# Kernel tuning notes

Hardware: AMD Instinct MI355X
Metric: run time of the kernel (lower is better)

## Reference

```python
import jax, jax.numpy as jnp
import numpy as np

N, T, F, H = 20000, 64, 32, 64
E = 640000
G1, G2 = 64, 32


def _lstm_layer(x_seq, Wih, Whh, bih, bhh):
    # x_seq: [N, T, Fin] -> hs [N, T, H], PyTorch gate order i,f,g,o
    n, _, _ = x_seq.shape
    h_dim = Whh.shape[1]
    h0 = jnp.zeros((n, h_dim), x_seq.dtype)
    c0 = jnp.zeros((n, h_dim), x_seq.dtype)

    def step(carry, xt):
        h, c = carry
        gates = xt @ Wih.T + h @ Whh.T + bih + bhh
        i, f, g, o = jnp.split(gates, 4, axis=-1)
        c = jax.nn.sigmoid(f) * c + jax.nn.sigmoid(i) * jnp.tanh(g)
        h = jax.nn.sigmoid(o) * jnp.tanh(c)
        return (h, c), h

    (_, _), hs = jax.lax.scan(step, (h0, c0), jnp.swapaxes(x_seq, 0, 1))
    return jnp.swapaxes(hs, 0, 1)


def _gcn(h, src, dst, W, b):
    # GCNConv (PyG default): add self-loops, symmetric deg^-1/2 normalization
    n = h.shape[0]
    loop = jnp.arange(n)
    s = jnp.concatenate([src, loop])
    d = jnp.concatenate([dst, loop])
    deg = jax.ops.segment_sum(jnp.ones_like(d, dtype=h.dtype), d, num_segments=n)
    dinv = jnp.where(deg > 0, deg ** -0.5, 0.0)
    norm = dinv[s] * dinv[d]
    xw = h @ W                      # [n, out]
    msg = xw[s] * norm[:, None]     # gather on source nodes
    return jax.ops.segment_sum(msg, d, num_segments=n) + b


def setup_inputs() -> dict:
    key = jax.random.key(0)
    ks = jax.random.split(key, 16)
    s = 0.1
    inp = {
        "x": jax.random.normal(ks[0], (N, T, F), jnp.float32),
        "stock_ids": jax.random.randint(ks[1], (N,), 0, N),
        "edge_index": jax.random.randint(ks[2], (2, E), 0, N),
        # LSTM layer 0
        "Wih0": jax.random.normal(ks[3], (4 * H, F), jnp.float32) * s,
        "Whh0": jax.random.normal(ks[4], (4 * H, H), jnp.float32) * s,
        "bih0": jnp.zeros((4 * H,), jnp.float32),
        "bhh0": jnp.zeros((4 * H,), jnp.float32),
        # LSTM layer 1
        "Wih1": jax.random.normal(ks[5], (4 * H, H), jnp.float32) * s,
        "Whh1": jax.random.normal(ks[6], (4 * H, H), jnp.float32) * s,
        "bih1": jnp.zeros((4 * H,), jnp.float32),
        "bhh1": jnp.zeros((4 * H,), jnp.float32),
        # GCN layers
        "gcn1_W": jax.random.normal(ks[7], (H, G1), jnp.float32) * s,
        "gcn1_b": jnp.zeros((G1,), jnp.float32),
        "gcn2_W": jax.random.normal(ks[8], (G1, G2), jnp.float32) * s,
        "gcn2_b": jnp.zeros((G2,), jnp.float32),
        # head
        "fc_W": jax.random.normal(ks[9], (1, G2), jnp.float32) * s,
        "fc_b": jnp.zeros((1,), jnp.float32),
    }
    return inp


def reference(x, stock_ids, edge_index, Wih0, Whh0, bih0, bhh0,
              Wih1, Whh1, bih1, bhh1, gcn1_W, gcn1_b, gcn2_W, gcn2_b,
              fc_W, fc_b):
    # 2-layer LSTM (eval mode: inter-layer dropout is identity)
    h1 = _lstm_layer(x, Wih0, Whh0, bih0, bhh0)
    h2 = _lstm_layer(h1, Wih1, Whh1, bih1, bhh1)
    h = h2[:, -1, :]                              # [N, H]
    src, dst = edge_index[0], edge_index[1]
    g = jax.nn.relu(_gcn(h, src, dst, gcn1_W, gcn1_b))
    g = jax.nn.relu(_gcn(g, src, dst, gcn2_W, gcn2_b))
    node_features = g[stock_ids]                  # [B, 32]
    out = node_features @ fc_W.T + fc_b           # [B, 1]
    return out.squeeze(-1)
```

## Files before the change

### kernel.cpp

```cpp
#include <hip/hip_runtime.h>
#include <math.h>

#define TT 64
#define FF 32
#define HH 64
#define NN 16
#define GG1 64
#define GG2 32

typedef float f32x4 __attribute__((ext_vector_type(4)));
typedef short bf16x8 __attribute__((ext_vector_type(8)));

__device__ __forceinline__ float fexp2(float x){ return __builtin_amdgcn_exp2f(x); }
__device__ __forceinline__ float frcp (float x){ return __builtin_amdgcn_rcpf(x); }
#define L2E 1.442695041f
__device__ __forceinline__ float sigm_nb(float v, float nb){
  return frcp(1.0f + fexp2(fmaf(v, -L2E, nb)));
}
__device__ __forceinline__ float tanh_b(float v, float b2){
  return fmaf(-2.0f, frcp(1.0f + fexp2(fmaf(v, 2.0f*L2E, b2))), 1.0f);
}
__device__ __forceinline__ float tanh0(float v){
  return fmaf(-2.0f, frcp(1.0f + fexp2(2.0f*L2E*v)), 1.0f);
}

__device__ __forceinline__ float xor8(float v){
  int a = __builtin_bit_cast(int, v);
  int b = __builtin_amdgcn_update_dpp(0, a, 0x128, 0xF, 0xF, true);
  return __builtin_bit_cast(float, b);
}

__device__ __forceinline__ unsigned short bf16rn(float x){
  unsigned u = __builtin_bit_cast(unsigned, x);
  return (unsigned short)((u + 0x7FFFu + ((u >> 16) & 1u)) >> 16);
}
__device__ __forceinline__ void split2(float x, unsigned short& h, unsigned short& l){
  unsigned u = __builtin_bit_cast(unsigned, x);
  unsigned hr = (u + 0x7FFFu + ((u >> 16) & 1u)) & 0xFFFF0000u;
  h = (unsigned short)(hr >> 16);
  l = bf16rn(x - __builtin_bit_cast(float, hr));
}
__device__ __forceinline__ void split_pk(float a, float b, unsigned& hi2, unsigned& lo2){
  asm("v_cvt_pk_bf16_f32 %0, %1, %2" : "=v"(hi2) : "v"(a), "v"(b));
  float ha = __builtin_bit_cast(float, hi2 << 16);
  float hb = __builtin_bit_cast(float, hi2 & 0xFFFF0000u);
  float la = a - ha, lb = b - hb;
  asm("v_cvt_pk_bf16_f32 %0, %1, %2" : "=v"(lo2) : "v"(la), "v"(lb));
}

#define PIN(v) asm volatile("" : "+v"(v))
#define MFMA(acc, a, b) (acc) = __builtin_amdgcn_mfma_f32_16x16x32_bf16((a), (b), (acc), 0, 0, 0)

__device__ __forceinline__ void wsplit(const float* p, bf16x8& hi, bf16x8& lo){
  float4 a = *(const float4*)p;
  float4 b = *(const float4*)(p + 4);
  unsigned short h, s;
  split2(a.x,h,s); hi[0]=(short)h; lo[0]=(short)s;
  split2(a.y,h,s); hi[1]=(short)h; lo[1]=(short)s;
  split2(a.z,h,s); hi[2]=(short)h; lo[2]=(short)s;
  split2(a.w,h,s); hi[3]=(short)h; lo[3]=(short)s;
  split2(b.x,h,s); hi[4]=(short)h; lo[4]=(short)s;
  split2(b.y,h,s); hi[5]=(short)h; lo[5]=(short)s;
  split2(b.z,h,s); hi[6]=(short)h; lo[6]=(short)s;
  split2(b.w,h,s); hi[7]=(short)h; lo[7]=(short)s;
}

__global__ __launch_bounds__(512, 2)
void lstm_mfma(const float* __restrict__ x,
    const float* __restrict__ Wih0, const float* __restrict__ Whh0,
    const float* __restrict__ bih0, const float* __restrict__ bhh0,
    const float* __restrict__ Wih1, const float* __restrict__ Whh1,
    const float* __restrict__ bih1, const float* __restrict__ bhh1,
    float* __restrict__ hout, int n)
{
  const int tid = threadIdx.x;
  const int w   = tid >> 6;
  const int l   = tid & 63;
  const int lr  = l & 15;
  const int lg  = l >> 4;
  const int nA  = blockIdx.x * NN;
  int avail = n - nA; if (avail > NN) avail = NN;

  __shared__ short Ax[2][2][16][40];
  __shared__ short H0[2][2][16][88];
  __shared__ short H1[2][2][16][88];

  const int jm   = lr & 7;
  const bool lo8 = (lr < 8);
  const int col0 = lo8 ? (8*w + jm) : (64  + 8*w + jm);
  const int col1 = lo8 ? (128 + 8*w + jm) : (192 + 8*w + jm);

  bf16x8 W0h[2][3], W0l[2][3], W1h[2][4], W1l[2][4];
#pragma unroll
  for (int h = 0; h < 2; ++h){
    const int col = h ? col1 : col0;
    wsplit(Wih0 + col*FF + 8*lg,      W0h[h][0], W0l[h][0]);
    wsplit(Whh0 + col*HH + 8*lg,      W0h[h][1], W0l[h][1]);
    wsplit(Whh0 + col*HH + 32 + 8*lg, W0h[h][2], W0l[h][2]);
    wsplit(Wih1 + col*HH + 8*lg,      W1h[h][0], W1l[h][0]);
    wsplit(Wih1 + col*HH + 32 + 8*lg, W1h[h][1], W1l[h][1]);
    wsplit(Whh1 + col*HH + 8*lg,      W1h[h][2], W1l[h][2]);
    wsplit(Whh1 + col*HH + 32 + 8*lg, W1h[h][3], W1l[h][3]);
  }
#pragma unroll
  for (int h = 0; h < 2; ++h){
#pragma unroll
    for (int k = 0; k < 3; ++k){ PIN(W0h[h][k]); PIN(W0l[h][k]); }
#pragma unroll
    for (int k = 0; k < 4; ++k){ PIN(W1h[h][k]); PIN(W1l[h][k]); }
  }

  const int m  = 8*w + jm;
  const float nb_i0 = -L2E      * (bih0[m      ] + bhh0[m      ]);
  const float nb_f0 = -L2E      * (bih0[m +  64] + bhh0[m +  64]);
  const float b2_g0 =  2.0f*L2E * (bih0[m + 128] + bhh0[m + 128]);
  const float nb_o0 = -L2E      * (bih0[m + 192] + bhh0[m + 192]);
  const float nb_i1 = -L2E      * (bih1[m      ] + bhh1[m      ]);
  const float nb_f1 = -L2E      * (bih1[m +  64] + bhh1[m +  64]);
  const float b2_g1 =  2.0f*L2E * (bih1[m + 128] + bhh1[m + 128]);
  const float nb_o1 = -L2E      * (bih1[m + 192] + bhh1[m + 192]);

  {
    short* p0 = &H0[0][0][0][0];
    short* p1 = &H1[0][0][0][0];
    for (int i = tid; i < 2*2*16*88; i += 512){ p0[i] = 0; p1[i] = 0; }
    const int xnd = tid >> 5, xf = tid & 31;
    float v = (xnd < avail) ? x[((size_t)(nA+xnd)*TT + 0)*FF + xf] : 0.0f;
    unsigned short hh, hl; split2(v, hh, hl);
    Ax[0][0][xnd][xf] = (short)hh;
    Ax[0][1][xnd][xf] = (short)hl;
  }
  const int na = 4*lg + (lo8 ? 0 : 2);
  const int nb = na + 1;
  float c0a = 0.0f, c0b = 0.0f, c1a = 0.0f, c1b = 0.0f;
  const f32x4 Z = {0.f, 0.f, 0.f, 0.f};
  __syncthreads();

  for (int t = 0; t < TT; ++t){
    const int rd0 = (t & 1) ^ 1;
    const int wr0 =  t & 1;
    const int rd1 =  t & 1;
    const int wr1 = (t & 1) ^ 1;

    const int xnd = tid >> 5, xf = tid & 31;
    const int tp = t + 1;
    float xv = 0.0f;
    if (tp < TT && xnd < avail) xv = x[((size_t)(nA+xnd)*TT + tp)*FF + xf];

    bf16x8 axh  = *(const bf16x8*)&Ax[t&1][0][lr][8*lg];
    bf16x8 axl  = *(const bf16x8*)&Ax[t&1][1][lr][8*lg];
    bf16x8 h0ah = *(const bf16x8*)&H0[rd0][0][lr][8*lg];
    bf16x8 h0al = *(const bf16x8*)&H0[rd0][1][lr][8*lg];
    bf16x8 h0bh = *(const bf16x8*)&H0[rd0][0][lr][32+8*lg];
    bf16x8 h0bl = *(const bf16x8*)&H0[rd0][1][lr][32+8*lg];

    __builtin_amdgcn_s_setprio(1);
    f32x4 acc0, acc1;
    acc0 = __builtin_amdgcn_mfma_f32_16x16x32_bf16(axl, W0h[0][0], Z, 0, 0, 0);
    acc1 = __builtin_amdgcn_mfma_f32_16x16x32_bf16(axl, W0h[1][0], Z, 0, 0, 0);
    MFMA(acc0, axh,  W0l[0][0]); MFMA(acc0, axh,  W0h[0][0]);
    MFMA(acc1, axh,  W0l[1][0]); MFMA(acc1, axh,  W0h[1][0]);
    MFMA(acc0, h0al, W0h[0][1]); MFMA(acc0, h0ah, W0l[0][1]); MFMA(acc0, h0ah, W0h[0][1]);
    MFMA(acc1, h0al, W0h[1][1]); MFMA(acc1, h0ah, W0l[1][1]); MFMA(acc1, h0ah, W0h[1][1]);
    MFMA(acc0, h0bl, W0h[0][2]); MFMA(acc0, h0bh, W0l[0][2]); MFMA(acc0, h0bh, W0h[0][2]);
    MFMA(acc1, h0bl, W0h[1][2]); MFMA(acc1, h0bh, W0l[1][2]); MFMA(acc1, h0bh, W0h[1][2]);

    f32x4 acd0, acd1;
    if (t > 0){
      bf16x8 h1ah = *(const bf16x8*)&H1[rd1][0][lr][8*lg];
      bf16x8 h1al = *(const bf16x8*)&H1[rd1][1][lr][8*lg];
      bf16x8 h1bh = *(const bf16x8*)&H1[rd1][0][lr][32+8*lg];
      bf16x8 h1bl = *(const bf16x8*)&H1[rd1][1][lr][32+8*lg];
      acd0 = __builtin_amdgcn_mfma_f32_16x16x32_bf16(h0al, W1h[0][0], Z, 0, 0, 0);
      acd1 = __builtin_amdgcn_mfma_f32_16x16x32_bf16(h0al, W1h[1][0], Z, 0, 0, 0);
      MFMA(acd0, h0ah, W1l[0][0]); MFMA(acd0, h0ah, W1h[0][0]);
      MFMA(acd1, h0ah, W1l[1][0]); MFMA(acd1, h0ah, W1h[1][0]);
      MFMA(acd0, h0bl, W1h[0][1]); MFMA(acd0, h0bh, W1l[0][1]); MFMA(acd0, h0bh, W1h[0][1]);
      MFMA(acd1, h0bl, W1h[1][1]); MFMA(acd1, h0bh, W1l[1][1]); MFMA(acd1, h0bh, W1h[1][1]);
      MFMA(acd0, h1al, W1h[0][2]); MFMA(acd0, h1ah, W1l[0][2]); MFMA(acd0, h1ah, W1h[0][2]);
      MFMA(acd1, h1al, W1h[1][2]); MFMA(acd1, h1ah, W1l[1][2]); MFMA(acd1, h1ah, W1h[1][2]);
      MFMA(acd0, h1bl, W1h[0][3]); MFMA(acd0, h1bh, W1l[0][3]); MFMA(acd0, h1bh, W1h[0][3]);
      MFMA(acd1, h1bl, W1h[1][3]); MFMA(acd1, h1bh, W1l[1][3]); MFMA(acd1, h1bh, W1h[1][3]);
    }
    __builtin_amdgcn_s_setprio(0);

    if (tp < TT){
      unsigned short hh, hl; split2(xv, hh, hl);
      Ax[tp&1][0][xnd][xf] = (short)hh;
      Ax[tp&1][1][xnd][xf] = (short)hl;
    }

    {
      f32x4 s0, s1;
      s0[0]=xor8(acc0[0]); s0[1]=xor8(acc0[1]); s0[2]=xor8(acc0[2]); s0[3]=xor8(acc0[3]);
      s1[0]=xor8(acc1[0]); s1[1]=xor8(acc1[1]); s1[2]=xor8(acc1[2]); s1[3]=xor8(acc1[3]);
      float gi_a = lo8 ? acc0[0] : s0[2],  gi_b = lo8 ? acc0[1] : s0[3];
      float gf_a = lo8 ? s0[0] : acc0[2],  gf_b = lo8 ? s0[1] : acc0[3];
      float gg_a = lo8 ? acc1[0] : s1[2],  gg_b = lo8 ? acc1[1] : s1[3];
      float go_a = lo8 ? s1[0] : acc1[2],  go_b = lo8 ? s1[1] : acc1[3];
      c0a = sigm_nb(gf_a, nb_f0)*c0a + sigm_nb(gi_a, nb_i0)*tanh_b(gg_a, b2_g0);
      float ha = sigm_nb(go_a, nb_o0)*tanh0(c0a);
      c0b = sigm_nb(gf_b, nb_f0)*c0b + sigm_nb(gi_b, nb_i0)*tanh_b(gg_b, b2_g0);
      float hb = sigm_nb(go_b, nb_o0)*tanh0(c0b);
      unsigned hi2, lo2; split_pk(ha, hb, hi2, lo2);
      H0[wr0][0][na][m] = (short)(hi2 & 0xFFFF);
      H0[wr0][0][nb][m] = (short)(hi2 >> 16);
      H0[wr0][1][na][m] = (short)(lo2 & 0xFFFF);
      H0[wr0][1][nb][m] = (short)(lo2 >> 16);
    }
    if (t > 0){
      f32x4 s0, s1;
      s0[0]=xor8(acd0[0]); s0[1]=xor8(acd0[1]); s0[2]=xor8(acd0[2]); s0[3]=xor8(acd0[3]);
      s1[0]=xor8(acd1[0]); s1[1]=xor8(acd1[1]); s1[2]=xor8(acd1[2]); s1[3]=xor8(acd1[3]);
      float gi_a = lo8 ? acd0[0] : s0[2],  gi_b = lo8 ? acd0[1] : s0[3];
      float gf_a = lo8 ? s0[0] : acd0[2],  gf_b = lo8 ? s0[1] : acd0[3];
      float gg_a = lo8 ? acd1[0] : s1[2],  gg_b = lo8 ? acd1[1] : s1[3];
      float go_a = lo8 ? s1[0] : acd1[2],  go_b = lo8 ? s1[1] : acd1[3];
      c1a = sigm_nb(gf_a, nb_f1)*c1a + sigm_nb(gi_a, nb_i1)*tanh_b(gg_a, b2_g1);
      float ha = sigm_nb(go_a, nb_o1)*tanh0(c1a);
      c1b = sigm_nb(gf_b, nb_f1)*c1b + sigm_nb(gi_b, nb_i1)*tanh_b(gg_b, b2_g1);
      float hb = sigm_nb(go_b, nb_o1)*tanh0(c1b);
      unsigned hi2, lo2; split_pk(ha, hb, hi2, lo2);
      H1[wr1][0][na][m] = (short)(hi2 & 0xFFFF);
      H1[wr1][0][nb][m] = (short)(hi2 >> 16);
      H1[wr1][1][na][m] = (short)(lo2 & 0xFFFF);
      H1[wr1][1][nb][m] = (short)(lo2 >> 16);
    }
    __syncthreads();
  }

  {
    const int rd0 = (TT-1) & 1;
    const int rd1 =  TT & 1;
    bf16x8 h0ah = *(const bf16x8*)&H0[rd0][0][lr][8*lg];
    bf16x8 h0al = *(const bf16x8*)&H0[rd0][1][lr][8*lg];
    bf16x8 h0bh = *(const bf16x8*)&H0[rd0][0][lr][32+8*lg];
    bf16x8 h0bl = *(const bf16x8*)&H0[rd0][1][lr][32+8*lg];
    bf16x8 h1ah = *(const bf16x8*)&H1[rd1][0][lr][8*lg];
    bf16x8 h1al = *(const bf16x8*)&H1[rd1][1][lr][8*lg];
    bf16x8 h1bh = *(const bf16x8*)&H1[rd1][0][lr][32+8*lg];
    bf16x8 h1bl = *(const bf16x8*)&H1[rd1][1][lr][32+8*lg];
    f32x4 acd0 = __builtin_amdgcn_mfma_f32_16x16x32_bf16(h0al, W1h[0][0], Z, 0, 0, 0);
    f32x4 acd1 = __builtin_amdgcn_mfma_f32_16x16x32_bf16(h0al, W1h[1][0], Z, 0, 0, 0);
    MFMA(acd0, h0ah, W1l[0][0]); MFMA(acd0, h0ah, W1h[0][0]);
    MFMA(acd1, h0ah, W1l[1][0]); MFMA(acd1, h0ah, W1h[1][0]);
    MFMA(acd0, h0bl, W1h[0][1]); MFMA(acd0, h0bh, W1l[0][1]); MFMA(acd0, h0bh, W1h[0][1]);
    MFMA(acd1, h0bl, W1h[1][1]); MFMA(acd1, h0bh, W1l[1][1]); MFMA(acd1, h0bh, W1h[1][1]);
    MFMA(acd0, h1al, W1h[0][2]); MFMA(acd0, h1ah, W1l[0][2]); MFMA(acd0, h1ah, W1h[0][2]);
    MFMA(acd1, h1al, W1h[1][2]); MFMA(acd1, h1ah, W1l[1][2]); MFMA(acd1, h1ah, W1h[1][2]);
    MFMA(acd0, h1bl, W1h[0][3]); MFMA(acd0, h1bh, W1l[0][3]); MFMA(acd0, h1bh, W1h[0][3]);
    MFMA(acd1, h1bl, W1h[1][3]); MFMA(acd1, h1bh, W1l[1][3]); MFMA(acd1, h1bh, W1h[1][3]);

    f32x4 s0, s1;
    s0[0]=xor8(acd0[0]); s0[1]=xor8(acd0[1]); s0[2]=xor8(acd0[2]); s0[3]=xor8(acd0[3]);
    s1[0]=xor8(acd1[0]); s1[1]=xor8(acd1[1]); s1[2]=xor8(acd1[2]); s1[3]=xor8(acd1[3]);
    float gi_a = lo8 ? acd0[0] : s0[2],  gi_b = lo8 ? acd0[1] : s0[3];
    float gf_a = lo8 ? s0[0] : acd0[2],  gf_b = lo8 ? s0[1] : acd0[3];
    float gg_a = lo8 ? acd1[0] : s1[2],  gg_b = lo8 ? acd1[1] : s1[3];
    float go_a = lo8 ? s1[0] : acd1[2],  go_b = lo8 ? s1[1] : acd1[3];
    c1a = sigm_nb(gf_a, nb_f1)*c1a + sigm_nb(gi_a, nb_i1)*tanh_b(gg_a, b2_g1);
    float ha = sigm_nb(go_a, nb_o1)*tanh0(c1a);
    c1b = sigm_nb(gf_b, nb_f1)*c1b + sigm_nb(gi_b, nb_i1)*tanh_b(gg_b, b2_g1);
    float hb = sigm_nb(go_b, nb_o1)*tanh0(c1b);
    if (nA + na < n) hout[(size_t)(nA+na)*HH + m] = ha;
    if (nA + nb < n) hout[(size_t)(nA+nb)*HH + m] = hb;
  }
}

__global__ void k_count(const int* __restrict__ dst, int E, int* __restrict__ cnt)
{
  int e = blockIdx.x * blockDim.x + threadIdx.x;
  if (e < E) atomicAdd(&cnt[dst[e]], 1);
}

__global__ void k_scan_build(const int* __restrict__ cnt, int n,
                             int* __restrict__ offs, int* __restrict__ cursor,
                             float* __restrict__ dinv)
{
  __shared__ int part[1024];
  const int tid = threadIdx.x;
  const int per = (n + 1023) >> 10;
  const int base = tid * per;
  int s = 0;
  for (int i = 0; i < per; ++i) { int idx = base + i; if (idx < n) s += cnt[idx]; }
  part[tid] = s;
  __syncthreads();
  for (int off = 1; off < 1024; off <<= 1) {
    int v = 0;
    if (tid >= off) v = part[tid - off];
    __syncthreads();
    part[tid] += v;
    __syncthreads();
  }
  int run = part[tid] - s;
  for (int i = 0; i < per; ++i) {
    int idx = base + i;
    if (idx < n) {
      offs[idx] = run; cursor[idx] = run;
      int c = cnt[idx];
      dinv[idx] = 1.0f / sqrtf((float)(c + 1));
      run += c;
    }
  }
}

__global__ void k_fill(const int* __restrict__ src, const int* __restrict__ dst,
                       int E, int* __restrict__ cursor, int* __restrict__ csr)
{
  int e = blockIdx.x * blockDim.x + threadIdx.x;
  if (e < E) {
    int d = dst[e];
    int pos = atomicAdd(&cursor[d], 1);
    csr[pos] = src[e];
  }
}

template <int K, int M>
__global__ void k_xw(const float* __restrict__ A, const float* __restrict__ W,
                     float* __restrict__ out, int n)
{
  int idx = blockIdx.x * blockDim.x + threadIdx.x;
  int row = idx / M, col = idx % M;
  if (row >= n) return;
  const float* a = A + (size_t)row * K;
  float acc = 0.0f;
#pragma unroll
  for (int k = 0; k < K; ++k) acc = fmaf(a[k], W[k*M + col], acc);
  out[(size_t)row*M + col] = acc;
}

__global__ void k_agg_x2(const float* __restrict__ xw, const int* __restrict__ offs,
                         const int* __restrict__ cnt, const int* __restrict__ csr,
                         const float* __restrict__ dinv, const float* __restrict__ b,
                         const float* __restrict__ W2,
                         float* __restrict__ g1out, float* __restrict__ xw2out, int n)
{
  __shared__ float sg[4][GG1];
  const int nd   = threadIdx.x >> 6;
  const int lane = threadIdx.x & 63;
  const int node = blockIdx.x * 4 + nd;
  if (node < n) {
    const float di = dinv[node];
    float acc = xw[(size_t)node*GG1 + lane] * di * di;
    const int s0 = offs[node], e0 = s0 + cnt[node];
    for (int p = s0; p < e0; ++p) {
      int s = csr[p];
      acc = fmaf(xw[(size_t)s*GG1 + lane], dinv[s] * di, acc);
    }
    float val = fmaxf(acc + b[lane], 0.0f);
    g1out[(size_t)node*GG1 + lane] = val;
    sg[nd][lane] = val;
  }
  __syncthreads();
  if (node < n && lane < GG2) {
    float a2 = 0.0f;
#pragma unroll
    for (int k = 0; k < GG1; ++k) a2 = fmaf(sg[nd][k], W2[k*GG2 + lane], a2);
    xw2out[(size_t)node*GG2 + lane] = a2;
  }
}

template <int FD>
__global__ void k_agg(const float* __restrict__ xw, const int* __restrict__ offs,
                      const int* __restrict__ cnt, const int* __restrict__ csr,
                      const float* __restrict__ dinv, const float* __restrict__ b,
                      float* __restrict__ out, int n)
{
  int gidx = blockIdx.x * blockDim.x + threadIdx.x;
  int node = gidx / FD, lane = gidx % FD;
  if (node >= n) return;
  const float di = dinv[node];
  float acc = xw[(size_t)node*FD + lane] * di * di;
  const int s0 = offs[node], e0 = s0 + cnt[node];
  for (int p = s0; p < e0; ++p) {
    int s = csr[p];
    acc = fmaf(xw[(size_t)s*FD + lane], dinv[s] * di, acc);
  }
  out[(size_t)node*FD + lane] = fmaxf(acc + b[lane], 0.0f);
}

__global__ void k_fc(const float* __restrict__ g2, const int* __restrict__ sid,
                     const float* __restrict__ fcW, const float* __restrict__ fcb,
                     float* __restrict__ out, int n)
{
  int i = blockIdx.x * blockDim.x + threadIdx.x;
  if (i >= n) return;
  const float* row = g2 + (size_t)sid[i] * GG2;
  float acc = fcb[0];
#pragma unroll
  for (int f = 0; f < GG2; ++f) acc = fmaf(row[f], fcW[f], acc);
  out[i] = acc;
}

extern "C" void kernel_launch(void* const* d_in, const int* in_sizes, int n_in,
                              void* d_out, int out_size, void* d_ws, size_t ws_size,
                              hipStream_t stream)
{
  const float* x    = (const float*)d_in[0];
  const int*   sid  = (const int*)  d_in[1];
  const int*   eidx = (const int*)  d_in[2];
  const float* Wih0 = (const float*)d_in[3];
  const float* Whh0 = (const float*)d_in[4];
  const float* bih0 = (const float*)d_in[5];
  const float* bhh0 = (const float*)d_in[6];
  const float* Wih1 = (const float*)d_in[7];
  const float* Whh1 = (const float*)d_in[8];
  const float* bih1 = (const float*)d_in[9];
  const float* bhh1 = (const float*)d_in[10];
  const float* g1W  = (const float*)d_in[11];
  const float* g1b  = (const float*)d_in[12];
  const float* g2W  = (const float*)d_in[13];
  const float* g2b  = (const float*)d_in[14];
  const float* fcW  = (const float*)d_in[15];
  const float* fcb  = (const float*)d_in[16];

  const int n = in_sizes[1];
  const int E = in_sizes[2] / 2;
  float* out = (float*)d_out;

  char* w = (char*)d_ws;
  auto carve = [&](size_t bytes) -> void* {
    void* p = (void*)w; w += (bytes + 255) & ~(size_t)255; return p;
  };
  float* hfin   = (float*)carve((size_t)n * HH * 4);
  int*   cnt    = (int*)  carve((size_t)n * 4);
  int*   offs   = (int*)  carve((size_t)n * 4);
  int*   cursor = (int*)  carve((size_t)n * 4);
  float* dinv   = (float*)carve((size_t)n * 4);
  int*   csr    = (int*)  carve((size_t)E * 4);
  float* xw1    = (float*)carve((size_t)n * GG1 * 4);
  float* g1     = (float*)carve((size_t)n * GG1 * 4);
  float* xw2    = (float*)carve((size_t)n * GG2 * 4);
  float* g2     = (float*)carve((size_t)n * GG2 * 4);

  const int* src = eidx;
  const int* dst = eidx + E;

  lstm_mfma<<<(n + NN - 1) / NN, 512, 0, stream>>>(x, Wih0, Whh0, bih0, bhh0,
                                                   Wih1, Whh1, bih1, bhh1, hfin, n);

  hipMemsetAsync(cnt, 0, (size_t)n * 4, stream);
  k_count<<<(E + 255) / 256, 256, 0, stream>>>(dst, E, cnt);
  k_scan_build<<<1, 1024, 0, stream>>>(cnt, n, offs, cursor, dinv);
  k_fill<<<(E + 255) / 256, 256, 0, stream>>>(src, dst, E, cursor, csr);

  k_xw<HH, GG1><<<((size_t)n * GG1 + 255) / 256, 256, 0, stream>>>(hfin, g1W, xw1, n);
  k_agg_x2<<<(n + 3) / 4, 256, 0, stream>>>(xw1, offs, cnt, csr, dinv, g1b, g2W, g1, xw2, n);

  k_agg<GG2><<<((size_t)n * GG2 + 255) / 256, 256, 0, stream>>>(xw2, offs, cnt, csr, dinv, g2b, g2, n);

  k_fc<<<(n + 255) / 256, 256, 0, stream>>>(g2, sid, fcW, fcb, out, n);
}
```

Before: 696.5 us.

## Split LSTM layers across two wave groups in a 1024-thread block

The LSTM kernel now launches 1024 threads per block. Waves 0-7 compute layer 0 and waves 8-15 compute layer 1 (time-skewed by one step), so each wave holds only one layer's split weights in registers instead of both. This cuts per-thread register pressure and lets the two layers' MFMA chains run on different waves concurrently rather than serially in the same wave. The costs are a larger block barrier across 16 waves each step, and a tighter launch-bounds target (1024 threads, 4 blocks) that may force spills.

```diff
diff --git a/kernel.cpp b/kernel.cpp
--- a/kernel.cpp
+++ b/kernel.cpp
@@ -65,7 +65,7 @@
   split2(b.w,h,s); hi[7]=(short)h; lo[7]=(short)s;
 }
 
-__global__ __launch_bounds__(512, 2)
+__global__ __launch_bounds__(1024, 4)
 void lstm_mfma(const float* __restrict__ x,
     const float* __restrict__ Wih0, const float* __restrict__ Whh0,
     const float* __restrict__ bih0, const float* __restrict__ bhh0,
@@ -73,12 +73,14 @@
     const float* __restrict__ bih1, const float* __restrict__ bhh1,
     float* __restrict__ hout, int n)
 {
-  const int tid = threadIdx.x;
-  const int w   = tid >> 6;
-  const int l   = tid & 63;
-  const int lr  = l & 15;
-  const int lg  = l >> 4;
-  const int nA  = blockIdx.x * NN;
+  const int tid  = threadIdx.x;
+  const int wv   = tid >> 6;
+  const int role = wv >> 3;
+  const int w    = wv & 7;
+  const int l    = tid & 63;
+  const int lr   = l & 15;
+  const int lg   = l >> 4;
+  const int nA   = blockIdx.x * NN;
   int avail = n - nA; if (avail > NN) avail = NN;
 
   __shared__ short Ax[2][2][16][40];
@@ -90,49 +92,54 @@
   const int col0 = lo8 ? (8*w + jm) : (64  + 8*w + jm);
   const int col1 = lo8 ? (128 + 8*w + jm) : (192 + 8*w + jm);
 
-  bf16x8 W0h[2][3], W0l[2][3], W1h[2][4], W1l[2][4];
-#pragma unroll
-  for (int h = 0; h < 2; ++h){
-    const int col = h ? col1 : col0;
-    wsplit(Wih0 + col*FF + 8*lg,      W0h[h][0], W0l[h][0]);
-    wsplit(Whh0 + col*HH + 8*lg,      W0h[h][1], W0l[h][1]);
-    wsplit(Whh0 + col*HH + 32 + 8*lg, W0h[h][2], W0l[h][2]);
-    wsplit(Wih1 + col*HH + 8*lg,      W1h[h][0], W1l[h][0]);
-    wsplit(Wih1 + col*HH + 32 + 8*lg, W1h[h][1], W1l[h][1]);
-    wsplit(Whh1 + col*HH + 8*lg,      W1h[h][2], W1l[h][2]);
-    wsplit(Whh1 + col*HH + 32 + 8*lg, W1h[h][3], W1l[h][3]);
-  }
-#pragma unroll
-  for (int h = 0; h < 2; ++h){
-#pragma unroll
-    for (int k = 0; k < 3; ++k){ PIN(W0h[h][k]); PIN(W0l[h][k]); }
-#pragma unroll
-    for (int k = 0; k < 4; ++k){ PIN(W1h[h][k]); PIN(W1l[h][k]); }
-  }
-
-  const int m  = 8*w + jm;
-  const float nb_i0 = -L2E      * (bih0[m      ] + bhh0[m      ]);
-  const float nb_f0 = -L2E      * (bih0[m +  64] + bhh0[m +  64]);
-  const float b2_g0 =  2.0f*L2E * (bih0[m + 128] + bhh0[m + 128]);
-  const float nb_o0 = -L2E      * (bih0[m + 192] + bhh0[m + 192]);
-  const float nb_i1 = -L2E      * (bih1[m      ] + bhh1[m      ]);
-  const float nb_f1 = -L2E      * (bih1[m +  64] + bhh1[m +  64]);
-  const float b2_g1 =  2.0f*L2E * (bih1[m + 128] + bhh1[m + 128]);
-  const float nb_o1 = -L2E      * (bih1[m + 192] + bhh1[m + 192]);
+  bf16x8 Wh[2][4], Wl[2][4];
+  if (role == 0){
+#pragma unroll
+    for (int h = 0; h < 2; ++h){
+      const int col = h ? col1 : col0;
+      wsplit(Wih0 + col*FF + 8*lg,      Wh[h][0], Wl[h][0]);
+      wsplit(Whh0 + col*HH + 8*lg,      Wh[h][1], Wl[h][1]);
+      wsplit(Whh0 + col*HH + 32 + 8*lg, Wh[h][2], Wl[h][2]);
+      Wh[h][3] = Wh[h][2]; Wl[h][3] = Wl[h][2];
+    }
+  } else {
+#pragma unroll
+    for (int h = 0; h < 2; ++h){
+      const int col = h ? col1 : col0;
+      wsplit(Wih1 + col*HH + 8*lg,      Wh[h][0], Wl[h][0]);
+      wsplit(Wih1 + col*HH + 32 + 8*lg, Wh[h][1], Wl[h][1]);
+      wsplit(Whh1 + col*HH + 8*lg,      Wh[h][2], Wl[h][2]);
+      wsplit(Whh1 + col*HH + 32 + 8*lg, Wh[h][3], Wl[h][3]);
+    }
+  }
+#pragma unroll
+  for (int h = 0; h < 2; ++h)
+#pragma unroll
+    for (int k = 0; k < 4; ++k){ PIN(Wh[h][k]); PIN(Wl[h][k]); }
+
+  const int m = 8*w + jm;
+  const float* bi = role ? bih1 : bih0;
+  const float* bh = role ? bhh1 : bhh0;
+  const float nb_i = -L2E      * (bi[m      ] + bh[m      ]);
+  const float nb_f = -L2E      * (bi[m +  64] + bh[m +  64]);
+  const float b2_g =  2.0f*L2E * (bi[m + 128] + bh[m + 128]);
+  const float nb_o = -L2E      * (bi[m + 192] + bh[m + 192]);
 
   {
     short* p0 = &H0[0][0][0][0];
     short* p1 = &H1[0][0][0][0];
-    for (int i = tid; i < 2*2*16*88; i += 512){ p0[i] = 0; p1[i] = 0; }
-    const int xnd = tid >> 5, xf = tid & 31;
-    float v = (xnd < avail) ? x[((size_t)(nA+xnd)*TT + 0)*FF + xf] : 0.0f;
-    unsigned short hh, hl; split2(v, hh, hl);
-    Ax[0][0][xnd][xf] = (short)hh;
-    Ax[0][1][xnd][xf] = (short)hl;
+    for (int i = tid; i < 2*2*16*88; i += 1024){ p0[i] = 0; p1[i] = 0; }
+    if (tid < 512){
+      const int xnd = tid >> 5, xf = tid & 31;
+      float v = (xnd < avail) ? x[((size_t)(nA+xnd)*TT + 0)*FF + xf] : 0.0f;
+      unsigned short hh, hl; split2(v, hh, hl);
+      Ax[0][0][xnd][xf] = (short)hh;
+      Ax[0][1][xnd][xf] = (short)hl;
+    }
   }
   const int na = 4*lg + (lo8 ? 0 : 2);
   const int nb = na + 1;
-  float c0a = 0.0f, c0b = 0.0f, c1a = 0.0f, c1b = 0.0f;
+  float ca = 0.0f, cb = 0.0f;
   const f32x4 Z = {0.f, 0.f, 0.f, 0.f};
   __syncthreads();
 
@@ -142,84 +149,89 @@
     const int rd1 =  t & 1;
     const int wr1 = (t & 1) ^ 1;
 
-    const int xnd = tid >> 5, xf = tid & 31;
-    const int tp = t + 1;
-    float xv = 0.0f;
-    if (tp < TT && xnd < avail) xv = x[((size_t)(nA+xnd)*TT + tp)*FF + xf];
-
-    bf16x8 axh  = *(const bf16x8*)&Ax[t&1][0][lr][8*lg];
-    bf16x8 axl  = *(const bf16x8*)&Ax[t&1][1][lr][8*lg];
-    bf16x8 h0ah = *(const bf16x8*)&H0[rd0][0][lr][8*lg];
-    bf16x8 h0al = *(const bf16x8*)&H0[rd0][1][lr][8*lg];
-    bf16x8 h0bh = *(const bf16x8*)&H0[rd0][0][lr][32+8*lg];
-    bf16x8 h0bl = *(const bf16x8*)&H0[rd0][1][lr][32+8*lg];
-
-    __builtin_amdgcn_s_setprio(1);
-    f32x4 acc0, acc1;
-    acc0 = __builtin_amdgcn_mfma_f32_16x16x32_bf16(axl, W0h[0][0], Z, 0, 0, 0);
-    acc1 = __builtin_amdgcn_mfma_f32_16x16x32_bf16(axl, W0h[1][0], Z, 0, 0, 0);
-    MFMA(acc0, axh,  W0l[0][0]); MFMA(acc0, axh,  W0h[0][0]);
-    MFMA(acc1, axh,  W0l[1][0]); MFMA(acc1, axh,  W0h[1][0]);
-    MFMA(acc0, h0al, W0h[0][1]); MFMA(acc0, h0ah, W0l[0][1]); MFMA(acc0, h0ah, W0h[0][1]);
-    MFMA(acc1, h0al, W0h[1][1]); MFMA(acc1, h0ah, W0l[1][1]); MFMA(acc1, h0ah, W0h[1][1]);
-    MFMA(acc0, h0bl, W0h[0][2]); MFMA(acc0, h0bh, W0l[0][2]); MFMA(acc0, h0bh, W0h[0][2]);
-    MFMA(acc1, h0bl, W0h[1][2]); MFMA(acc1, h0bh, W0l[1][2]); MFMA(acc1, h0bh, W0h[1][2]);
-
-    f32x4 acd0, acd1;
-    if (t > 0){
-      bf16x8 h1ah = *(const bf16x8*)&H1[rd1][0][lr][8*lg];
-      bf16x8 h1al = *(const bf16x8*)&H1[rd1][1][lr][8*lg];
-      bf16x8 h1bh = *(const bf16x8*)&H1[rd1][0][lr][32+8*lg];
-      bf16x8 h1bl = *(const bf16x8*)&H1[rd1][1][lr][32+8*lg];
-      acd0 = __builtin_amdgcn_mfma_f32_16x16x32_bf16(h0al, W1h[0][0], Z, 0, 0, 0);
-      acd1 = __builtin_amdgcn_mfma_f32_16x16x32_bf16(h0al, W1h[1][0], Z, 0, 0, 0);
-      MFMA(acd0, h0ah, W1l[0][0]); MFMA(acd0, h0ah, W1h[0][0]);
-      MFMA(acd1, h0ah, W1l[1][0]); MFMA(acd1, h0ah, W1h[1][0]);
-      MFMA(acd0, h0bl, W1h[0][1]); MFMA(acd0, h0bh, W1l[0][1]); MFMA(acd0, h0bh, W1h[0][1]);
-      MFMA(acd1, h0bl, W1h[1][1]); MFMA(acd1, h0bh, W1l[1][1]); MFMA(acd1, h0bh, W1h[1][1]);
-      MFMA(acd0, h1al, W1h[0][2]); MFMA(acd0, h1ah, W1l[0][2]); MFMA(acd0, h1ah, W1h[0][2]);
-      MFMA(acd1, h1al, W1h[1][2]); MFMA(acd1, h1ah, W1l[1][2]); MFMA(acd1, h1ah, W1h[1][2]);
-      MFMA(acd0, h1bl, W1h[0][3]); MFMA(acd0, h1bh, W1l[0][3]); MFMA(acd0, h1bh, W1h[0][3]);
-      MFMA(acd1, h1bl, W1h[1][3]); MFMA(acd1, h1bh, W1l[1][3]); MFMA(acd1, h1bh, W1h[1][3]);
-    }
-    __builtin_amdgcn_s_setprio(0);
-
-    if (tp < TT){
-      unsigned short hh, hl; split2(xv, hh, hl);
-      Ax[tp&1][0][xnd][xf] = (short)hh;
-      Ax[tp&1][1][xnd][xf] = (short)hl;
-    }
-
-    {
+    if (role == 0){
+      const int xnd = tid >> 5, xf = tid & 31;
+      const int tp = t + 1;
+      float xv = 0.0f;
+      if (tp < TT && xnd < avail) xv = x[((size_t)(nA+xnd)*TT + tp)*FF + xf];
+
+      bf16x8 axh  = *(const bf16x8*)&Ax[t&1][0][lr][8*lg];
+      bf16x8 axl  = *(const bf16x8*)&Ax[t&1][1][lr][8*lg];
+      bf16x8 h0ah = *(const bf16x8*)&H0[rd0][0][lr][8*lg];
+      bf16x8 h0al = *(const bf16x8*)&H0[rd0][1][lr][8*lg];
+      bf16x8 h0bh = *(const bf16x8*)&H0[rd0][0][lr][32+8*lg];
+      bf16x8 h0bl = *(const bf16x8*)&H0[rd0][1][lr][32+8*lg];
+
+      __builtin_amdgcn_s_setprio(1);
+      f32x4 A0, A1;
+      A0 = __builtin_amdgcn_mfma_f32_16x16x32_bf16(axl, Wh[0][0], Z, 0, 0, 0);
+      A1 = __builtin_amdgcn_mfma_f32_16x16x32_bf16(axl, Wh[1][0], Z, 0, 0, 0);
+      MFMA(A0, axh,  Wl[0][0]); MFMA(A0, axh,  Wh[0][0]);
+      MFMA(A1, axh,  Wl[1][0]); MFMA(A1, axh,  Wh[1][0]);
+      MFMA(A0, h0al, Wh[0][1]); MFMA(A0, h0ah, Wl[0][1]); MFMA(A0, h0ah, Wh[0][1]);
+      MFMA(A1, h0al, Wh[1][1]); MFMA(A1, h0ah, Wl[1][1]); MFMA(A1, h0ah, Wh[1][1]);
+      MFMA(A0, h0bl, Wh[0][2]); MFMA(A0, h0bh, Wl[0][2]); MFMA(A0, h0bh, Wh[0][2]);
+      MFMA(A1, h0bl, Wh[1][2]); MFMA(A1, h0bh, Wl[1][2]); MFMA(A1, h0bh, Wh[1][2]);
+      __builtin_amdgcn_s_setprio(0);
+
+      if (tp < TT){
+        unsigned short hh, hl; split2(xv, hh, hl);
+        Ax[tp&1][0][xnd][xf] = (short)hh;
+        Ax[tp&1][1][xnd][xf] = (short)hl;
+      }
+
       f32x4 s0, s1;
-      s0[0]=xor8(acc0[0]); s0[1]=xor8(acc0[1]); s0[2]=xor8(acc0[2]); s0[3]=xor8(acc0[3]);
-      s1[0]=xor8(acc1[0]); s1[1]=xor8(acc1[1]); s1[2]=xor8(acc1[2]); s1[3]=xor8(acc1[3]);
-      float gi_a = lo8 ? acc0[0] : s0[2],  gi_b = lo8 ? acc0[1] : s0[3];
-      float gf_a = lo8 ? s0[0] : acc0[2],  gf_b = lo8 ? s0[1] : acc0[3];
-      float gg_a = lo8 ? acc1[0] : s1[2],  gg_b = lo8 ? acc1[1] : s1[3];
-      float go_a = lo8 ? s1[0] : acc1[2],  go_b = lo8 ? s1[1] : acc1[3];
-      c0a = sigm_nb(gf_a, nb_f0)*c0a + sigm_nb(gi_a, nb_i0)*tanh_b(gg_a, b2_g0);
-      float ha = sigm_nb(go_a, nb_o0)*tanh0(c0a);
-      c0b = sigm_nb(gf_b, nb_f0)*c0b + sigm_nb(gi_b, nb_i0)*tanh_b(gg_b, b2_g0);
-      float hb = sigm_nb(go_b, nb_o0)*tanh0(c0b);
+      s0[0]=xor8(A0[0]); s0[1]=xor8(A0[1]); s0[2]=xor8(A0[2]); s0[3]=xor8(A0[3]);
+      s1[0]=xor8(A1[0]); s1[1]=xor8(A1[1]); s1[2]=xor8(A1[2]); s1[3]=xor8(A1[3]);
+      float gi_a = lo8 ? A0[0] : s0[2],  gi_b = lo8 ? A0[1] : s0[3];
+      float gf_a = lo8 ? s0[0] : A0[2],  gf_b = lo8 ? s0[1] : A0[3];
+      float gg_a = lo8 ? A1[0] : s1[2],  gg_b = lo8 ? A1[1] : s1[3];
+      float go_a = lo8 ? s1[0] : A1[2],  go_b = lo8 ? s1[1] : A1[3];
+      ca = sigm_nb(gf_a, nb_f)*ca + sigm_nb(gi_a, nb_i)*tanh_b(gg_a, b2_g);
+      float ha = sigm_nb(go_a, nb_o)*tanh0(ca);
+      cb = sigm_nb(gf_b, nb_f)*cb + sigm_nb(gi_b, nb_i)*tanh_b(gg_b, b2_g);
+      float hb = sigm_nb(go_b, nb_o)*tanh0(cb);
       unsigned hi2, lo2; split_pk(ha, hb, hi2, lo2);
       H0[wr0][0][na][m] = (short)(hi2 & 0xFFFF);
       H0[wr0][0][nb][m] = (short)(hi2 >> 16);
       H0[wr0][1][na][m] = (short)(lo2 & 0xFFFF);
       H0[wr0][1][nb][m] = (short)(lo2 >> 16);
     }
-    if (t > 0){
+    else if (t > 0){
+      bf16x8 h0ah = *(const bf16x8*)&H0[rd0][0][lr][8*lg];
+      bf16x8 h0al = *(const bf16x8*)&H0[rd0][1][lr][8*lg];
+      bf16x8 h0bh = *(const bf16x8*)&H0[rd0][0][lr][32+8*lg];
+      bf16x8 h0bl = *(const bf16x8*)&H0[rd0][1][lr][32+8*lg];
+
+      __builtin_amdgcn_s_setprio(1);
+      f32x4 D0, D1;
+      D0 = __builtin_amdgcn_mfma_f32_16x16x32_bf16(h0al, Wh[0][0], Z, 0, 0, 0);
+      D1 = __builtin_amdgcn_mfma_f32_16x16x32_bf16(h0al, Wh[1][0], Z, 0, 0, 0);
+      MFMA(D0, h0ah, Wl[0][0]); MFMA(D0, h0ah, Wh[0][0]);
+      MFMA(D1, h0ah, Wl[1][0]); MFMA(D1, h0ah, Wh[1][0]);
+      MFMA(D0, h0bl, Wh[0][1]); MFMA(D0, h0bh, Wl[0][1]); MFMA(D0, h0bh, Wh[0][1]);
+      MFMA(D1, h0bl, Wh[1][1]); MFMA(D1, h0bh, Wl[1][1]); MFMA(D1, h0bh, Wh[1][1]);
+      bf16x8 h1ah = *(const bf16x8*)&H1[rd1][0][lr][8*lg];
+      bf16x8 h1al = *(const bf16x8*)&H1[rd1][1][lr][8*lg];
+      bf16x8 h1bh = *(const bf16x8*)&H1[rd1][0][lr][32+8*lg];
+      bf16x8 h1bl = *(const bf16x8*)&H1[rd1][1][lr][32+8*lg];
+      MFMA(D0, h1al, Wh[0][2]); MFMA(D0, h1ah, Wl[0][2]); MFMA(D0, h1ah, Wh[0][2]);
+      MFMA(D1, h1al, Wh[1][2]); MFMA(D1, h1ah, Wl[1][2]); MFMA(D1, h1ah, Wh[1][2]);
+      MFMA(D0, h1bl, Wh[0][3]); MFMA(D0, h1bh, Wl[0][3]); MFMA(D0, h1bh, Wh[0][3]);
+      MFMA(D1, h1bl, Wh[1][3]); MFMA(D1, h1bh, Wl[1][3]); MFMA(D1, h1bh, Wh[1][3]);
+      __builtin_amdgcn_s_setprio(0);
+
       f32x4 s0, s1;
-      s0[0]=xor8(acd0[0]); s0[1]=xor8(acd0[1]); s0[2]=xor8(acd0[2]); s0[3]=xor8(acd0[3]);
-      s1[0]=xor8(acd1[0]); s1[1]=xor8(acd1[1]); s1[2]=xor8(acd1[2]); s1[3]=xor8(acd1[3]);
-      float gi_a = lo8 ? acd0[0] : s0[2],  gi_b = lo8 ? acd0[1] : s0[3];
-      float gf_a = lo8 ? s0[0] : acd0[2],  gf_b = lo8 ? s0[1] : acd0[3];
-      float gg_a = lo8 ? acd1[0] : s1[2],  gg_b = lo8 ? acd1[1] : s1[3];
-      float go_a = lo8 ? s1[0] : acd1[2],  go_b = lo8 ? s1[1] : acd1[3];
-      c1a = sigm_nb(gf_a, nb_f1)*c1a + sigm_nb(gi_a, nb_i1)*tanh_b(gg_a, b2_g1);
-      float ha = sigm_nb(go_a, nb_o1)*tanh0(c1a);
-      c1b = sigm_nb(gf_b, nb_f1)*c1b + sigm_nb(gi_b, nb_i1)*tanh_b(gg_b, b2_g1);
-      float hb = sigm_nb(go_b, nb_o1)*tanh0(c1b);
+      s0[0]=xor8(D0[0]); s0[1]=xor8(D0[1]); s0[2]=xor8(D0[2]); s0[3]=xor8(D0[3]);
+      s1[0]=xor8(D1[0]); s1[1]=xor8(D1[1]); s1[2]=xor8(D1[2]); s1[3]=xor8(D1[3]);
+      float gi_a = lo8 ? D0[0] : s0[2],  gi_b = lo8 ? D0[1] : s0[3];
+      float gf_a = lo8 ? s0[0] : D0[2],  gf_b = lo8 ? s0[1] : D0[3];
+      float gg_a = lo8 ? D1[0] : s1[2],  gg_b = lo8 ? D1[1] : s1[3];
+      float go_a = lo8 ? s1[0] : D1[2],  go_b = lo8 ? s1[1] : D1[3];
+      ca = sigm_nb(gf_a, nb_f)*ca + sigm_nb(gi_a, nb_i)*tanh_b(gg_a, b2_g);
+      float ha = sigm_nb(go_a, nb_o)*tanh0(ca);
+      cb = sigm_nb(gf_b, nb_f)*cb + sigm_nb(gi_b, nb_i)*tanh_b(gg_b, b2_g);
+      float hb = sigm_nb(go_b, nb_o)*tanh0(cb);
       unsigned hi2, lo2; split_pk(ha, hb, hi2, lo2);
       H1[wr1][0][na][m] = (short)(hi2 & 0xFFFF);
       H1[wr1][0][nb][m] = (short)(hi2 >> 16);
@@ -229,7 +241,7 @@
     __syncthreads();
   }
 
-  {
+  if (role == 1){
     const int rd0 = (TT-1) & 1;
     const int rd1 =  TT & 1;
     bf16x8 h0ah = *(const bf16x8*)&H0[rd0][0][lr][8*lg];
@@ -240,28 +252,28 @@
     bf16x8 h1al = *(const bf16x8*)&H1[rd1][1][lr][8*lg];
     bf16x8 h1bh = *(const bf16x8*)&H1[rd1][0][lr][32+8*lg];
     bf16x8 h1bl = *(const bf16x8*)&H1[rd1][1][lr][32+8*lg];
-    f32x4 acd0 = __builtin_amdgcn_mfma_f32_16x16x32_bf16(h0al, W1h[0][0], Z, 0, 0, 0);
-    f32x4 acd1 = __builtin_amdgcn_mfma_f32_16x16x32_bf16(h0al, W1h[1][0], Z, 0, 0, 0);
-    MFMA(acd0, h0ah, W1l[0][0]); MFMA(acd0, h0ah, W1h[0][0]);
-    MFMA(acd1, h0ah, W1l[1][0]); MFMA(acd1, h0ah, W1h[1][0]);
-    MFMA(acd0, h0bl, W1h[0][1]); MFMA(acd0, h0bh, W1l[0][1]); MFMA(acd0, h0bh, W1h[0][1]);
-    MFMA(acd1, h0bl, W1h[1][1]); MFMA(acd1, h0bh, W1l[1][1]); MFMA(acd1, h0bh, W1h[1][1]);
-    MFMA(acd0, h1al, W1h[0][2]); MFMA(acd0, h1ah, W1l[0][2]); MFMA(acd0, h1ah, W1h[0][2]);
-    MFMA(acd1, h1al, W1h[1][2]); MFMA(acd1, h1ah, W1l[1][2]); MFMA(acd1, h1ah, W1h[1][2]);
-    MFMA(acd0, h1bl, W1h[0][3]); MFMA(acd0, h1bh, W1l[0][3]); MFMA(acd0, h1bh, W1h[0][3]);
-    MFMA(acd1, h1bl, W1h[1][3]); MFMA(acd1, h1bh, W1l[1][3]); MFMA(acd1, h1bh, W1h[1][3]);
+    f32x4 D0 = __builtin_amdgcn_mfma_f32_16x16x32_bf16(h0al, Wh[0][0], Z, 0, 0, 0);
+    f32x4 D1 = __builtin_amdgcn_mfma_f32_16x16x32_bf16(h0al, Wh[1][0], Z, 0, 0, 0);
+    MFMA(D0, h0ah, Wl[0][0]); MFMA(D0, h0ah, Wh[0][0]);
+    MFMA(D1, h0ah, Wl[1][0]); MFMA(D1, h0ah, Wh[1][0]);
+    MFMA(D0, h0bl, Wh[0][1]); MFMA(D0, h0bh, Wl[0][1]); MFMA(D0, h0bh, Wh[0][1]);
+    MFMA(D1, h0bl, Wh[1][1]); MFMA(D1, h0bh, Wl[1][1]); MFMA(D1, h0bh, Wh[1][1]);
+    MFMA(D0, h1al, Wh[0][2]); MFMA(D0, h1ah, Wl[0][2]); MFMA(D0, h1ah, Wh[0][2]);
+    MFMA(D1, h1al, Wh[1][2]); MFMA(D1, h1ah, Wl[1][2]); MFMA(D1, h1ah, Wh[1][2]);
+    MFMA(D0, h1bl, Wh[0][3]); MFMA(D0, h1bh, Wl[0][3]); MFMA(D0, h1bh, Wh[0][3]);
+    MFMA(D1, h1bl, Wh[1][3]); MFMA(D1, h1bh, Wl[1][3]); MFMA(D1, h1bh, Wh[1][3]);
 
     f32x4 s0, s1;
-    s0[0]=xor8(acd0[0]); s0[1]=xor8(acd0[1]); s0[2]=xor8(acd0[2]); s0[3]=xor8(acd0[3]);
-    s1[0]=xor8(acd1[0]); s1[1]=xor8(acd1[1]); s1[2]=xor8(acd1[2]); s1[3]=xor8(acd1[3]);
-    float gi_a = lo8 ? acd0[0] : s0[2],  gi_b = lo8 ? acd0[1] : s0[3];
-    float gf_a = lo8 ? s0[0] : acd0[2],  gf_b = lo8 ? s0[1] : acd0[3];
-    float gg_a = lo8 ? acd1[0] : s1[2],  gg_b = lo8 ? acd1[1] : s1[3];
-    float go_a = lo8 ? s1[0] : acd1[2],  go_b = lo8 ? s1[1] : acd1[3];
-    c1a = sigm_nb(gf_a, nb_f1)*c1a + sigm_nb(gi_a, nb_i1)*tanh_b(gg_a, b2_g1);
-    float ha = sigm_nb(go_a, nb_o1)*tanh0(c1a);
-    c1b = sigm_nb(gf_b, nb_f1)*c1b + sigm_nb(gi_b, nb_i1)*tanh_b(gg_b, b2_g1);
-    float hb = sigm_nb(go_b, nb_o1)*tanh0(c1b);
+    s0[0]=xor8(D0[0]); s0[1]=xor8(D0[1]); s0[2]=xor8(D0[2]); s0[3]=xor8(D0[3]);
+    s1[0]=xor8(D1[0]); s1[1]=xor8(D1[1]); s1[2]=xor8(D1[2]); s1[3]=xor8(D1[3]);
+    float gi_a = lo8 ? D0[0] : s0[2],  gi_b = lo8 ? D0[1] : s0[3];
+    float gf_a = lo8 ? s0[0] : D0[2],  gf_b = lo8 ? s0[1] : D0[3];
+    float gg_a = lo8 ? D1[0] : s1[2],  gg_b = lo8 ? D1[1] : s1[3];
+    float go_a = lo8 ? s1[0] : D1[2],  go_b = lo8 ? s1[1] : D1[3];
+    ca = sigm_nb(gf_a, nb_f)*ca + sigm_nb(gi_a, nb_i)*tanh_b(gg_a, b2_g);
+    float ha = sigm_nb(go_a, nb_o)*tanh0(ca);
+    cb = sigm_nb(gf_b, nb_f)*cb + sigm_nb(gi_b, nb_i)*tanh_b(gg_b, b2_g);
+    float hb = sigm_nb(go_b, nb_o)*tanh0(cb);
     if (nA + na < n) hout[(size_t)(nA+na)*HH + m] = ha;
     if (nA + nb < n) hout[(size_t)(nA+nb)*HH + m] = hb;
   }
@@ -436,8 +448,8 @@
   const int* src = eidx;
   const int* dst = eidx + E;
 
-  lstm_mfma<<<(n + NN - 1) / NN, 512, 0, stream>>>(x, Wih0, Whh0, bih0, bhh0,
-                                                   Wih1, Whh1, bih1, bhh1, hfin, n);
+  lstm_mfma<<<(n + NN - 1) / NN, 1024, 0, stream>>>(x, Wih0, Whh0, bih0, bhh0,
+                                                    Wih1, Whh1, bih1, bhh1, hfin, n);
 
   hipMemsetAsync(cnt, 0, (size_t)n * 4, stream);
   k_count<<<(E + 255) / 256, 256, 0, stream>>>(dst, E, cnt);
```

New measurement: 683.4 us. Within noise of the previous version (-1.9%).
